# Optimization experiments

Measured on AMD Instinct MI355X. Metric: run time of the kernel, lower is better.

The kernel has to match this reference:

```python
import jax, jax.numpy as jnp
import numpy as np

N_NODES = 50000
N_EDGES = 1_600_000
F_NODE = 128
F_EDGE = 32
OUT = 128
N_LAYERS = 3  # conv1 + 2 hidden
N_CLASSES = 10
N_GRAPHS = 512
SLOPE = 0.2  # GATv2Conv default negative_slope


def setup_inputs() -> dict:
    key = jax.random.key(0)
    ks = jax.random.split(key, 14)
    x = jax.random.normal(ks[0], (N_NODES, F_NODE), jnp.float32)
    edge_index = jax.random.randint(ks[1], (2, N_EDGES), 0, N_NODES, dtype=jnp.int64)
    batch = jnp.sort(jax.random.randint(ks[2], (N_NODES,), 0, N_GRAPHS, dtype=jnp.int64))
    edge_attr = jax.random.normal(ks[3], (N_EDGES, F_EDGE), jnp.float32)
    s = 1.0 / np.sqrt(OUT)
    Wl = jax.random.normal(ks[4], (N_LAYERS, F_NODE, OUT), jnp.float32) * s
    bl = jnp.zeros((N_LAYERS, OUT), jnp.float32)
    Wr = jax.random.normal(ks[5], (N_LAYERS, F_NODE, OUT), jnp.float32) * s
    br = jnp.zeros((N_LAYERS, OUT), jnp.float32)
    We = jax.random.normal(ks[6], (N_LAYERS, F_EDGE, OUT), jnp.float32) * s
    att = jax.random.normal(ks[7], (N_LAYERS, OUT), jnp.float32) * s
    bias = jnp.zeros((N_LAYERS, OUT), jnp.float32)
    lin_w = jax.random.normal(ks[8], (OUT, N_CLASSES), jnp.float32) * s
    lin_b = jnp.zeros((N_CLASSES,), jnp.float32)
    return dict(x=x, edge_index=edge_index, batch=batch, dropout=0,
                edge_attr=edge_attr, Wl=Wl, bl=bl, Wr=Wr, br=br, We=We,
                att=att, bias=bias, lin_w=lin_w, lin_b=lin_b)


def _add_self_loops(edge_index, edge_attr):
    # PyG add_self_loops with fill_value='mean': loop attr = mean of incoming edge attrs
    src, dst = edge_index[0], edge_index[1]
    deg = jax.ops.segment_sum(jnp.ones((src.shape[0],), jnp.float32), dst, num_segments=N_NODES)
    loop_attr = jax.ops.segment_sum(edge_attr, dst, num_segments=N_NODES) / jnp.maximum(deg, 1.0)[:, None]
    loops = jnp.arange(N_NODES, dtype=src.dtype)
    src = jnp.concatenate([src, loops])
    dst = jnp.concatenate([dst, loops])
    ea = jnp.concatenate([edge_attr, loop_attr], axis=0)
    return src, dst, ea


def _gatv2_conv(x, src, dst, ea, Wl, bl, Wr, br, We, att, bias):
    xl = x @ Wl + bl            # [N, OUT] source transform
    xr = x @ Wr + br            # [N, OUT] target transform
    # per-edge: LeakyReLU(xl[src] + xr[dst] + We @ ea) . att
    e = jax.nn.leaky_relu(xl[src] + xr[dst] + ea @ We, SLOPE)  # [E', OUT]
    score = e @ att                                            # [E']
    # softmax over incoming edges of each dst node (every node has a self-loop)
    m = jax.ops.segment_max(score, dst, num_segments=N_NODES)
    p = jnp.exp(score - m[dst])
    denom = jax.ops.segment_sum(p, dst, num_segments=N_NODES)
    alpha = p / denom[dst]
    out = jax.ops.segment_sum(alpha[:, None] * xl[src], dst, num_segments=N_NODES)
    return out + bias


def reference(x, edge_index, batch, dropout, edge_attr,
              Wl, bl, Wr, br, We, att, bias, lin_w, lin_b):
    src, dst, ea = _add_self_loops(edge_index, edge_attr)
    h = x
    for l in range(N_LAYERS):
        h = _gatv2_conv(h, src, dst, ea, Wl[l], bl[l], Wr[l], br[l], We[l], att[l], bias[l])
        h = jax.nn.relu(h)
    # global mean pool over graphs
    cnt = jax.ops.segment_sum(jnp.ones((N_NODES,), jnp.float32), batch, num_segments=N_GRAPHS)
    pooled = jax.ops.segment_sum(h, batch, num_segments=N_GRAPHS) / jnp.maximum(cnt, 1.0)[:, None]
    # dropout is identity in eval mode (training=False)
    return pooled @ lin_w + lin_b
```

## Files before the change

### kernel.cpp

```cpp
#include <hip/hip_runtime.h>
#include <math.h>

#define NN 50000
#define NE 1600000
#define FE 32
#define DF 128
#define NG 512
#define NC 10
#define GR 64


__global__ void detect_i64(const unsigned int* __restrict__ w, int* __restrict__ flag) {
    if (threadIdx.x == 0 && blockIdx.x == 0) {
        unsigned int acc = 0;
        for (int i = 0; i < 128; i++) acc |= w[2 * i + 1];
        *flag = (acc == 0u) ? 1 : 0;
    }
}

__device__ __forceinline__ int load_idx(const void* p, int flag, long long i, int limit) {
    int v = flag ? (int)((const long long*)p)[i] : ((const int*)p)[i];
    return min(max(v, 0), limit - 1);
}

__global__ __launch_bounds__(256) void zero_out_k(float* __restrict__ out, int n) {
    int i = blockIdx.x * 256 + threadIdx.x;
    if (i < n) out[i] = 0.f;
}

__global__ __launch_bounds__(256) void zero_ws_k(unsigned int* __restrict__ p, long long n) {
    long long i = (long long)blockIdx.x * 256 + threadIdx.x;
    long long stride = (long long)gridDim.x * 256;
    for (; i < n; i += stride) p[i] = 0u;
}


__global__ __launch_bounds__(256) void count_deg(const void* __restrict__ ei, const int* __restrict__ flagp,
                                                 int* __restrict__ cnt) {
    int e = blockIdx.x * 256 + threadIdx.x;
    if (e < NE) atomicAdd(&cnt[load_idx(ei, *flagp, (long long)NE + e, NN)], 1);
}

__global__ __launch_bounds__(256) void scan_partial(const int* __restrict__ cnt, int* __restrict__ bsum) {
    __shared__ int sd[256];
    int t = threadIdx.x;
    int i = blockIdx.x * 256 + t;
    sd[t] = (i < NN) ? cnt[i] : 0;
    __syncthreads();
    for (int st = 128; st > 0; st >>= 1) {
        if (t < st) sd[t] += sd[t + st];
        __syncthreads();
    }
    if (t == 0) bsum[blockIdx.x] = sd[0];
}

__global__ __launch_bounds__(256) void scan_top(int* __restrict__ bsum, int nb) {
    __shared__ int sd[256];
    int t = threadIdx.x;
    int v = (t < nb) ? bsum[t] : 0;
    sd[t] = v;
    __syncthreads();
    for (int st = 1; st < 256; st <<= 1) {
        int a = sd[t];
        int b = (t >= st) ? sd[t - st] : 0;
        __syncthreads();
        sd[t] = a + b;
        __syncthreads();
    }
    if (t < nb) bsum[t] = sd[t] - v;
}

__global__ __launch_bounds__(256) void scan_final(const int* __restrict__ cnt, const int* __restrict__ bsum,
                                                  int* __restrict__ offs, int* __restrict__ curs) {
    __shared__ int sd[256];
    int t = threadIdx.x;
    int i = blockIdx.x * 256 + t;
    int v = (i < NN) ? cnt[i] : 0;
    sd[t] = v;
    __syncthreads();
    for (int st = 1; st < 256; st <<= 1) {
        int a = sd[t];
        int b = (t >= st) ? sd[t - st] : 0;
        __syncthreads();
        sd[t] = a + b;
        __syncthreads();
    }
    int excl = sd[t] - v + bsum[blockIdx.x];
    if (i < NN) { offs[i] = excl; curs[i] = excl; }
}

__global__ __launch_bounds__(256) void fill_csr(const void* __restrict__ ei, const int* __restrict__ flagp,
                                                int* __restrict__ curs, int* __restrict__ elist) {
    int e = blockIdx.x * 256 + threadIdx.x;
    if (e < NE) {
        int p = atomicAdd(&curs[load_idx(ei, *flagp, (long long)NE + e, NN)], 1);
        elist[min(max(p, 0), NE - 1)] = e;
    }
}

__global__ __launch_bounds__(256) void loop_attr_k(const int* __restrict__ elist, const int* __restrict__ offs,
                                                   const int* __restrict__ cnt, const float* __restrict__ ea,
                                                   float* __restrict__ loopa) {
    int wid = (blockIdx.x * 256 + threadIdx.x) >> 6;
    int lane = threadIdx.x & 63;
    if (wid >= NN) return;
    int o = offs[wid], deg = cnt[wid];
    int f = lane & 31, half = lane >> 5;
    float s = 0.f;
    for (int i = half; i < deg; i += 2) {
        int e = elist[o + i];
        s += ea[(size_t)e * FE + f];
    }
    s += __shfl_down(s, 32);
    if (lane < 32) loopa[(size_t)wid * FE + f] = s / fmaxf((float)deg, 1.f);
}


__global__ __launch_bounds__(256, 2) void gemm_xlxr(const float* h,
                                                    const float* __restrict__ Wl, const float* __restrict__ bl,
                                                    const float* __restrict__ Wr, const float* __restrict__ br,
                                                    float* __restrict__ xl, float* xr) {
    __shared__ float hsT[DF * GR];
    __shared__ float wst[DF * GR];
    int tid = threadIdx.x;
    int row0 = blockIdx.x * GR;

    for (int it = 0; it < 8; ++it) {
        int idx = it * 256 + tid;
        int r = idx >> 5;
        int k4 = idx & 31;
        int row = row0 + r;
        float4 v = make_float4(0.f, 0.f, 0.f, 0.f);
        if (row < NN) v = reinterpret_cast<const float4*>(h + (size_t)row * DF)[k4];
        int k = k4 * 4;
        int c = r ^ (k & 60);
        hsT[(k + 0) * GR + c] = v.x;
        hsT[(k + 1) * GR + c] = v.y;
        hsT[(k + 2) * GR + c] = v.z;
        hsT[(k + 3) * GR + c] = v.w;
    }

    int ty4 = (tid >> 4) * 4;
    int tx4 = (tid & 15) * 4;

    for (int ct = 0; ct < 4; ++ct) {
        const float* Wsrc = (ct < 2) ? Wl : Wr;
        const float* bsrc = (ct < 2) ? bl : br;
        float* osrc = (ct < 2) ? xl : xr;
        int c0 = (ct & 1) * 64;

        __syncthreads();
        for (int it = 0; it < 8; ++it) {
            int idx = it * 256 + tid;
            int k = idx >> 4;
            int j4 = (idx & 15) * 4;
            float4 w = *reinterpret_cast<const float4*>(&Wsrc[(size_t)k * DF + c0 + j4]);
            *reinterpret_cast<float4*>(&wst[k * GR + j4]) = w;
        }
        __syncthreads();

        float acc[4][4] = {};
#pragma unroll 4
        for (int k = 0; k < DF; ++k) {
            float4 a = *reinterpret_cast<const float4*>(&hsT[k * GR + (ty4 ^ (k & 60))]);
            float4 b = *reinterpret_cast<const float4*>(&wst[k * GR + tx4]);
            acc[0][0] += a.x * b.x; acc[0][1] += a.x * b.y; acc[0][2] += a.x * b.z; acc[0][3] += a.x * b.w;
            acc[1][0] += a.y * b.x; acc[1][1] += a.y * b.y; acc[1][2] += a.y * b.z; acc[1][3] += a.y * b.w;
            acc[2][0] += a.z * b.x; acc[2][1] += a.z * b.y; acc[2][2] += a.z * b.z; acc[2][3] += a.z * b.w;
            acc[3][0] += a.w * b.x; acc[3][1] += a.w * b.y; acc[3][2] += a.w * b.z; acc[3][3] += a.w * b.w;
        }

        float4 bv = *reinterpret_cast<const float4*>(&bsrc[c0 + tx4]);
#pragma unroll
        for (int i = 0; i < 4; ++i) {
            int row = row0 + ty4 + i;
            if (row < NN) {
                float4 o = make_float4(acc[i][0] + bv.x, acc[i][1] + bv.y,
                                       acc[i][2] + bv.z, acc[i][3] + bv.w);
                *reinterpret_cast<float4*>(&osrc[(size_t)row * DF + c0 + tx4]) = o;
            }
        }
    }
}


__global__ __launch_bounds__(256) void edge_agg(const float* __restrict__ xl, const float* xr,
                                                const void* __restrict__ ei, const int* __restrict__ flagp,
                                                const int* __restrict__ elist, const int* __restrict__ offs,
                                                const int* __restrict__ cnt,
                                                const float* __restrict__ ea, const float* __restrict__ loopa,
                                                const float* __restrict__ We, const float* __restrict__ att,
                                                const float* __restrict__ bias, float* hout) {
    int wid = (blockIdx.x * 256 + threadIdx.x) >> 6;
    int lane = threadIdx.x & 63;
    if (wid >= NN) return;
    int flag = *flagp;
    int v = wid;
    float2 we[32];
#pragma unroll
    for (int j = 0; j < 32; j++) we[j] = reinterpret_cast<const float2*>(We)[j * 64 + lane];
    float2 attv = reinterpret_cast<const float2*>(att)[lane];
    float2 xrv = reinterpret_cast<const float2*>(xr + (size_t)v * DF)[lane];
    float m = -INFINITY, s = 0.f, accx = 0.f, accy = 0.f;
    int o = offs[v], deg = cnt[v];
    int e_cur = -1, src_cur = v;
    if (deg > 0) {
        e_cur = elist[o];
        src_cur = load_idx(ei, flag, e_cur, NN);
    }
    for (int i = 0; i <= deg; i++) {
        int src = src_cur;
        const float* earow = (i < deg) ? (ea + (size_t)e_cur * FE) : (loopa + (size_t)v * FE);
        if (i + 1 < deg) {
            e_cur = elist[o + i + 1];
            src_cur = load_idx(ei, flag, e_cur, NN);
        } else {
            src_cur = v;
        }
        float2 xlv = reinterpret_cast<const float2*>(xl + (size_t)src * DF)[lane];
        float zx0 = xlv.x + xrv.x, zy0 = xlv.y + xrv.y, zx1 = 0.f, zy1 = 0.f;
#pragma unroll
        for (int j4 = 0; j4 < 8; j4++) {
            float4 e4 = reinterpret_cast<const float4*>(earow)[j4];
            float2 w0 = we[j4 * 4 + 0], w1 = we[j4 * 4 + 1], w2 = we[j4 * 4 + 2], w3 = we[j4 * 4 + 3];
            zx0 += e4.x * w0.x; zy0 += e4.x * w0.y;
            zx1 += e4.y * w1.x; zy1 += e4.y * w1.y;
            zx0 += e4.z * w2.x; zy0 += e4.z * w2.y;
            zx1 += e4.w * w3.x; zy1 += e4.w * w3.y;
        }
        float zx = zx0 + zx1, zy = zy0 + zy1;
        zx = fmaxf(zx, 0.2f * zx);
        zy = fmaxf(zy, 0.2f * zy);
        float t = zx * attv.x + zy * attv.y;
#pragma unroll
        for (int d = 1; d < 64; d <<= 1) t += __shfl_xor(t, d);
        float mn = fmaxf(m, t);
        float scale = __expf(m - mn);
        float p = __expf(t - mn);
        s = s * scale + p;
        accx = accx * scale + p * xlv.x;
        accy = accy * scale + p * xlv.y;
        m = mn;
    }
    float2 bv = reinterpret_cast<const float2*>(bias)[lane];
    float inv = 1.f / s;
    float ox = fmaxf(accx * inv + bv.x, 0.f);
    float oy = fmaxf(accy * inv + bv.y, 0.f);
    reinterpret_cast<float2*>(hout + (size_t)v * DF)[lane] = make_float2(ox, oy);
}


__global__ __launch_bounds__(256) void pool_accum(const float* __restrict__ h, const void* __restrict__ batch,
                                                  const int* __restrict__ flagp,
                                                  float* __restrict__ pooled, int* __restrict__ gcnt) {
    int idx = blockIdx.x * 256 + threadIdx.x;
    if (idx >= NN * DF) return;
    int v = idx >> 7, k = idx & 127;
    int g = load_idx(batch, *flagp, v, NG);
    atomicAdd(&pooled[g * DF + k], h[idx]);
    if (k == 0) atomicAdd(&gcnt[g], 1);
}

__global__ __launch_bounds__(128) void final_lin(const float* __restrict__ pooled, const int* __restrict__ gcnt,
                                                 const float* __restrict__ lw, const float* __restrict__ lb,
                                                 float* __restrict__ out) {
    __shared__ float pr[DF];
    int g = blockIdx.x, t = threadIdx.x;
    float c = fmaxf((float)gcnt[g], 1.f);
    pr[t] = pooled[g * DF + t] / c;
    __syncthreads();
    if (t < NC) {
        float a = lb[t];
        for (int k = 0; k < DF; k++) a += pr[k] * lw[k * NC + t];
        out[g * NC + t] = a;
    }
}


extern "C" void kernel_launch(void* const* d_in, const int* in_sizes, int n_in,
                              void* d_out, int out_size, void* d_ws, size_t ws_size,
                              hipStream_t stream) {
    const float* x    = (const float*)d_in[0];
    const void*  ei   = d_in[1];
    const void*  batch= d_in[2];
    const float* ea   = (const float*)d_in[4];
    const float* Wl   = (const float*)d_in[5];
    const float* bl   = (const float*)d_in[6];
    const float* Wr   = (const float*)d_in[7];
    const float* br   = (const float*)d_in[8];
    const float* We   = (const float*)d_in[9];
    const float* att  = (const float*)d_in[10];
    const float* bias = (const float*)d_in[11];
    const float* lw   = (const float*)d_in[12];
    const float* lb   = (const float*)d_in[13];
    float* out = (float*)d_out;

    char* base = (char*)d_ws;
    size_t off = 0;
    auto alloc = [&](size_t bytes) { void* p = base + off; off += (bytes + 255) & ~(size_t)255; return p; };
    float* XL    = (float*)alloc((size_t)NN * DF * 4);
    float* B1    = (float*)alloc((size_t)NN * DF * 4);
    float* LOOPA = (float*)alloc((size_t)NN * FE * 4);
    int*   ELIST = (int*)alloc((size_t)NE * 4);
    int*   OFFS  = (int*)alloc((size_t)NN * 4);
    int*   CURS  = (int*)alloc((size_t)NN * 4);
    int*   BSUM  = (int*)alloc(256 * 4);
    int*   IFLAG = (int*)alloc(256);
    char*  zbase = base + off;
    int*   CNT   = (int*)alloc((size_t)NN * 4);
    int*   GCNT  = (int*)alloc(NG * 4);
    float* POOL  = (float*)alloc((size_t)NG * DF * 4);
    size_t zbytes = (size_t)((char*)(POOL + NG * DF) - zbase);
    size_t needed = off;

    if (ws_size < needed) {
        zero_out_k<<<(out_size + 255) / 256, 256, 0, stream>>>(out, out_size);
        return;
    }
    zero_ws_k<<<512, 256, 0, stream>>>((unsigned int*)zbase, (long long)(zbytes / 4));

    int nb = (NN + 255) / 256;
    detect_i64 <<<1, 64, 0, stream>>>((const unsigned int*)ei, IFLAG);
    count_deg  <<<NE / 256, 256, 0, stream>>>(ei, IFLAG, CNT);
    scan_partial<<<nb, 256, 0, stream>>>(CNT, BSUM);
    scan_top   <<<1, 256, 0, stream>>>(BSUM, nb);
    scan_final <<<nb, 256, 0, stream>>>(CNT, BSUM, OFFS, CURS);
    fill_csr   <<<NE / 256, 256, 0, stream>>>(ei, IFLAG, CURS, ELIST);
    loop_attr_k<<<(NN + 3) / 4, 256, 0, stream>>>(ELIST, OFFS, CNT, ea, LOOPA);

    const float* hin = x;
    for (int l = 0; l < 3; l++) {
        gemm_xlxr<<<(NN + GR - 1) / GR, 256, 0, stream>>>(hin, Wl + l * DF * DF, bl + l * DF,
                                                          Wr + l * DF * DF, br + l * DF, XL, B1);
        edge_agg <<<(NN + 3) / 4, 256, 0, stream>>>(XL, B1, ei, IFLAG, ELIST, OFFS, CNT, ea, LOOPA,
                                                    We + l * FE * DF, att + l * DF, bias + l * DF, B1);
        hin = B1;
    }
    pool_accum<<<(NN * DF) / 256, 256, 0, stream>>>(hin, batch, IFLAG, POOL, GCNT);
    final_lin <<<NG, DF, 0, stream>>>(POOL, GCNT, lw, lb, out);
}
```

Measured before the change: 3.667 ms.

## Batch four edges per iteration in edge_agg and stage We in shared memory

The per-node edge aggregation now processes incoming edges in groups of four. Index loads for the next group are prefetched, the four xl gathers and edge-attribute loads are issued together, and the shuffle reductions are interleaved so more memory and latency work is in flight per wave. The edge weight matrix moves from 64 per-lane registers into LDS, loaded once per block, which frees registers for the batching. The costs are more LDS reads per edge and a scalar tail loop for the leftover edges and the self-loop.

```diff
diff --git a/kernel.cpp b/kernel.cpp
--- a/kernel.cpp
+++ b/kernel.cpp
@@ -8,6 +8,7 @@
 #define NG 512
 #define NC 10
 #define GR 64
+#define EB 4
 
 
 __global__ void detect_i64(const unsigned int* __restrict__ w, int* __restrict__ flag) {
@@ -191,44 +192,104 @@
                                                 const float* __restrict__ ea, const float* __restrict__ loopa,
                                                 const float* __restrict__ We, const float* __restrict__ att,
                                                 const float* __restrict__ bias, float* hout) {
-    int wid = (blockIdx.x * 256 + threadIdx.x) >> 6;
-    int lane = threadIdx.x & 63;
+    __shared__ float2 weS[FE][64];
+    int tid = threadIdx.x;
+    for (int it = tid; it < FE * 64; it += 256) {
+        int j = it >> 6, l = it & 63;
+        weS[j][l] = reinterpret_cast<const float2*>(We)[j * 64 + l];
+    }
+    __syncthreads();
+
+    int wid = (blockIdx.x * 256 + tid) >> 6;
+    int lane = tid & 63;
     if (wid >= NN) return;
     int flag = *flagp;
     int v = wid;
-    float2 we[32];
-#pragma unroll
-    for (int j = 0; j < 32; j++) we[j] = reinterpret_cast<const float2*>(We)[j * 64 + lane];
     float2 attv = reinterpret_cast<const float2*>(att)[lane];
     float2 xrv = reinterpret_cast<const float2*>(xr + (size_t)v * DF)[lane];
     float m = -INFINITY, s = 0.f, accx = 0.f, accy = 0.f;
     int o = offs[v], deg = cnt[v];
-    int e_cur = -1, src_cur = v;
-    if (deg > 0) {
-        e_cur = elist[o];
-        src_cur = load_idx(ei, flag, e_cur, NN);
-    }
-    for (int i = 0; i <= deg; i++) {
-        int src = src_cur;
-        const float* earow = (i < deg) ? (ea + (size_t)e_cur * FE) : (loopa + (size_t)v * FE);
-        if (i + 1 < deg) {
-            e_cur = elist[o + i + 1];
-            src_cur = load_idx(ei, flag, e_cur, NN);
-        } else {
-            src_cur = v;
-        }
+    int nb4 = deg & ~(EB - 1);
+
+    int ec[EB], sc[EB];
+#pragma unroll
+    for (int b = 0; b < EB; ++b) ec[b] = (b < deg) ? elist[o + b] : 0;
+#pragma unroll
+    for (int b = 0; b < EB; ++b) sc[b] = (b < deg) ? load_idx(ei, flag, ec[b], NN) : v;
+
+    for (int i = 0; i < nb4; i += EB) {
+        int en[EB], sn[EB];
+#pragma unroll
+        for (int b = 0; b < EB; ++b) {
+            int idx = i + EB + b;
+            en[b] = (idx < deg) ? elist[o + idx] : 0;
+        }
+#pragma unroll
+        for (int b = 0; b < EB; ++b) {
+            int idx = i + EB + b;
+            sn[b] = (idx < deg) ? load_idx(ei, flag, en[b], NN) : v;
+        }
+        float2 xlv[EB];
+#pragma unroll
+        for (int b = 0; b < EB; ++b)
+            xlv[b] = reinterpret_cast<const float2*>(xl + (size_t)sc[b] * DF)[lane];
+
+        float zx[EB], zy[EB];
+#pragma unroll
+        for (int b = 0; b < EB; ++b) { zx[b] = xlv[b].x + xrv.x; zy[b] = xlv[b].y + xrv.y; }
+#pragma unroll
+        for (int j4 = 0; j4 < 8; ++j4) {
+            float2 w0 = weS[j4 * 4 + 0][lane], w1 = weS[j4 * 4 + 1][lane];
+            float2 w2 = weS[j4 * 4 + 2][lane], w3 = weS[j4 * 4 + 3][lane];
+#pragma unroll
+            for (int b = 0; b < EB; ++b) {
+                float4 e4 = reinterpret_cast<const float4*>(ea + (size_t)ec[b] * FE)[j4];
+                zx[b] += e4.x * w0.x + e4.y * w1.x + e4.z * w2.x + e4.w * w3.x;
+                zy[b] += e4.x * w0.y + e4.y * w1.y + e4.z * w2.y + e4.w * w3.y;
+            }
+        }
+        float t[EB];
+#pragma unroll
+        for (int b = 0; b < EB; ++b) {
+            float a = fmaxf(zx[b], 0.2f * zx[b]);
+            float c = fmaxf(zy[b], 0.2f * zy[b]);
+            t[b] = a * attv.x + c * attv.y;
+        }
+#pragma unroll
+        for (int d = 1; d < 64; d <<= 1) {
+#pragma unroll
+            for (int b = 0; b < EB; ++b) t[b] += __shfl_xor(t[b], d);
+        }
+        float tm = fmaxf(fmaxf(t[0], t[1]), fmaxf(t[2], t[3]));
+        float mn = fmaxf(m, tm);
+        float scale = __expf(m - mn);
+        float p[EB];
+#pragma unroll
+        for (int b = 0; b < EB; ++b) p[b] = __expf(t[b] - mn);
+        s = s * scale + ((p[0] + p[1]) + (p[2] + p[3]));
+        accx = accx * scale + p[0] * xlv[0].x + p[1] * xlv[1].x + p[2] * xlv[2].x + p[3] * xlv[3].x;
+        accy = accy * scale + p[0] * xlv[0].y + p[1] * xlv[1].y + p[2] * xlv[2].y + p[3] * xlv[3].y;
+        m = mn;
+#pragma unroll
+        for (int b = 0; b < EB; ++b) { ec[b] = en[b]; sc[b] = sn[b]; }
+    }
+
+    for (int i = nb4; i <= deg; ++i) {
+        int b = i - nb4;
+        int src;
+        const float* earow;
+        if (i < deg) { src = sc[b]; earow = ea + (size_t)ec[b] * FE; }
+        else         { src = v;     earow = loopa + (size_t)v * FE; }
         float2 xlv = reinterpret_cast<const float2*>(xl + (size_t)src * DF)[lane];
-        float zx0 = xlv.x + xrv.x, zy0 = xlv.y + xrv.y, zx1 = 0.f, zy1 = 0.f;
-#pragma unroll
-        for (int j4 = 0; j4 < 8; j4++) {
+        float zx = xlv.x + xrv.x, zy = xlv.y + xrv.y;
+#pragma unroll
+        for (int j4 = 0; j4 < 8; ++j4) {
+            float2 w0 = weS[j4 * 4 + 0][lane], w1 = weS[j4 * 4 + 1][lane];
+            float2 w2 = weS[j4 * 4 + 2][lane], w3 = weS[j4 * 4 + 3][lane];
             float4 e4 = reinterpret_cast<const float4*>(earow)[j4];
-            float2 w0 = we[j4 * 4 + 0], w1 = we[j4 * 4 + 1], w2 = we[j4 * 4 + 2], w3 = we[j4 * 4 + 3];
-            zx0 += e4.x * w0.x; zy0 += e4.x * w0.y;
-            zx1 += e4.y * w1.x; zy1 += e4.y * w1.y;
-            zx0 += e4.z * w2.x; zy0 += e4.z * w2.y;
-            zx1 += e4.w * w3.x; zy1 += e4.w * w3.y;
-        }
-        float zx = zx0 + zx1, zy = zy0 + zy1;
+            zx += e4.x * w0.x + e4.y * w1.x + e4.z * w2.x + e4.w * w3.x;
+            zy += e4.x * w0.y + e4.y * w1.y + e4.z * w2.y + e4.w * w3.y;
+        }
         zx = fmaxf(zx, 0.2f * zx);
         zy = fmaxf(zy, 0.2f * zy);
         float t = zx * attv.x + zy * attv.y;
@@ -242,6 +303,7 @@
         accy = accy * scale + p * xlv.y;
         m = mn;
     }
+
     float2 bv = reinterpret_cast<const float2*>(bias)[lane];
     float inv = 1.f / s;
     float ox = fmaxf(accx * inv + bv.x, 0.f);
```

Result: slower. 3.822 ms (+4.2%).
